# Optimization experiments

Hardware: AMD Instinct MI355X
Metric: run time of the kernel (lower is better)

The kernel has to match this reference:

```python
import jax, jax.numpy as jnp
import numpy as np

B, K, D = 4096, 16, 256
NUM_CODES = 512
BETA = 0.25  # commitment (activation_entropy=None path)
LN_EPS = 1e-5

def setup_inputs() -> dict:
    key = jax.random.key(0)
    ks = jax.random.split(key, 6)
    hidden = jax.random.normal(ks[0], (B, K, D), dtype=jnp.float32)
    active_mask = jax.random.randint(ks[1], (B, K), 0, 2).astype(bool)
    bound = 1.0 / NUM_CODES
    codebook = jax.random.uniform(ks[2], (NUM_CODES, D), minval=-bound, maxval=bound, dtype=jnp.float32)
    lim = 1.0 / np.sqrt(D)
    W_in = jax.random.uniform(ks[3], (D, D), minval=-lim, maxval=lim, dtype=jnp.float32)
    W_out = jax.random.uniform(ks[4], (D, D), minval=-lim, maxval=lim, dtype=jnp.float32)
    ln_gamma = jnp.ones((D,), jnp.float32)
    ln_beta = jnp.zeros((D,), jnp.float32)
    return {"hidden": hidden, "active_mask": active_mask, "codebook": codebook,
            "W_in": W_in, "W_out": W_out, "ln_gamma": ln_gamma, "ln_beta": ln_beta}

def reference(hidden, active_mask, codebook, W_in, W_out, ln_gamma, ln_beta):
    sg = jax.lax.stop_gradient
    z = jnp.einsum('bkd,ed->bke', hidden, W_in)              # proj_in (no bias)
    z_flat = z.reshape(-1, D)                                 # [B*K, D]
    # ||z - c||^2 = |z|^2 - 2 z.c + |c|^2
    dist = (jnp.sum(z_flat * z_flat, -1, keepdims=True)
            - 2.0 * z_flat @ codebook.T
            + jnp.sum(codebook * codebook, -1))               # [B*K, C]
    idx = jnp.argmin(dist, axis=-1)                           # [B*K]
    z_q = codebook[idx].reshape(z.shape)                      # gather
    vq_loss = jnp.mean((sg(z_q) - z) ** 2) + BETA * jnp.mean((z_q - sg(z)) ** 2)
    z_st = z + sg(z_q - z)                                    # straight-through
    out = jnp.einsum('bkd,ed->bke', z_st, W_out)              # proj_out
    h = hidden + active_mask[..., None].astype(jnp.float32) * out
    mu = jnp.mean(h, -1, keepdims=True)
    var = jnp.mean((h - mu) ** 2, -1, keepdims=True)
    h_comm = (h - mu) * jax.lax.rsqrt(var + LN_EPS) * ln_gamma + ln_beta
    return h_comm, vq_loss
```

## Files before the change

kernel.cpp:

```cpp
#include <hip/hip_runtime.h>

#define LN_EPS 1e-5f

typedef short bf16x8 __attribute__((ext_vector_type(8)));
typedef float f32x4  __attribute__((ext_vector_type(4)));

__device__ __forceinline__ unsigned short f2bf(float f) {
  unsigned u = __float_as_uint(f);
  u += 0x7fffu + ((u >> 16) & 1u);
  return (unsigned short)(u >> 16);
}
__device__ __forceinline__ float bf2f(unsigned short s) {
  return __uint_as_float(((unsigned)s) << 16);
}
__device__ __forceinline__ int swz(int r) { return (r ^ (r >> 2)) & 3; }

__device__ __forceinline__ bf16x8 pack8(float4 a, float4 b) {
  bf16x8 v;
  v[0] = (short)f2bf(a.x); v[1] = (short)f2bf(a.y);
  v[2] = (short)f2bf(a.z); v[3] = (short)f2bf(a.w);
  v[4] = (short)f2bf(b.x); v[5] = (short)f2bf(b.y);
  v[6] = (short)f2bf(b.z); v[7] = (short)f2bf(b.w);
  return v;
}

__device__ __forceinline__ void ldst16(const unsigned short* g, unsigned short* l) {
  __builtin_amdgcn_global_load_lds(
      (const __attribute__((address_space(1))) unsigned int*)g,
      (__attribute__((address_space(3))) unsigned int*)l, 16, 0, 0);
}

__global__ __launch_bounds__(256) void prep_kernel(
    const float* __restrict__ codebook, const float* __restrict__ W_in,
    const float* __restrict__ W_out,
    float* __restrict__ loss_acc, unsigned* __restrict__ ticket,
    float* __restrict__ c2, float* __restrict__ code_out,
    unsigned short* __restrict__ BT) {
  const int b = blockIdx.x, t = threadIdx.x;
  if (b < 32) {
    if (b == 0 && t == 0) { *loss_acc = 0.f; *ticket = 0u; }
    int e = b * 8 + (t >> 5);
    int c32 = t & 31, ks = c32 >> 2, kq = c32 & 3;
    const float* src = W_in + e * 256 + c32 * 8;
    float4 x0 = *(const float4*)src, x1 = *(const float4*)(src + 4);
    *(bf16x8*)(BT + ks * 8192 + e * 32 + ((kq ^ swz(e)) * 8)) = pack8(x0, x1);
  } else if (b < 96) {
    int code = (b - 32) * 8 + (t >> 5);
    int c32 = t & 31, ks = c32 >> 2, kq = c32 & 3;
    const float* src = codebook + code * 256 + c32 * 8;
    float4 x0 = *(const float4*)src, x1 = *(const float4*)(src + 4);
    int rl = code & 255;
    int chunk = 8 + (code >> 8) * 8 + ks;
    *(bf16x8*)(BT + chunk * 8192 + rl * 32 + ((kq ^ swz(rl)) * 8)) = pack8(x0, x1);
    float s = x0.x * x0.x + x0.y * x0.y + x0.z * x0.z + x0.w * x0.w +
              x1.x * x1.x + x1.y * x1.y + x1.z * x1.z + x1.w * x1.w;
    s += __shfl_xor(s, 1);  s += __shfl_xor(s, 2);
    s += __shfl_xor(s, 4);  s += __shfl_xor(s, 8);
    s += __shfl_xor(s, 16);
    if ((t & 31) == 0) c2[code] = s;
  } else {
    __shared__ float Cs[32][260];
    __shared__ float Ws[16][260];
    int bi = b - 96, ci = bi & 15, ei = bi >> 4;
    {
      int row = t >> 4, col = (t & 15) * 16;
      const float4* s = (const float4*)(W_out + (size_t)(ei * 16 + row) * 256 + col);
      float4* d = (float4*)&Ws[row][col];
      d[0] = s[0]; d[1] = s[1]; d[2] = s[2]; d[3] = s[3];
    }
    {
      int row = t >> 3, col = (t & 7) * 32;
      const float4* s = (const float4*)(codebook + (size_t)(ci * 32 + row) * 256 + col);
      float4* d = (float4*)&Cs[row][col];
      #pragma unroll
      for (int k = 0; k < 8; k++) d[k] = s[k];
    }
    __syncthreads();
    int c = t & 31, e0 = t >> 5;
    float a0 = 0.f, a1 = 0.f;
    #pragma unroll 4
    for (int d = 0; d < 256; d += 4) {
      float4 cv = *(const float4*)&Cs[c][d];
      float4 w0 = *(const float4*)&Ws[e0][d];
      float4 w1 = *(const float4*)&Ws[e0 + 8][d];
      a0 += cv.x * w0.x + cv.y * w0.y + cv.z * w0.z + cv.w * w0.w;
      a1 += cv.x * w1.x + cv.y * w1.y + cv.z * w1.z + cv.w * w1.w;
    }
    code_out[(size_t)(ci * 32 + c) * 256 + ei * 16 + e0]     = a0;
    code_out[(size_t)(ci * 32 + c) * 256 + ei * 16 + e0 + 8] = a1;
  }
}

__global__ __launch_bounds__(256, 2) void main_kernel(
    const float* __restrict__ hidden, const int* __restrict__ mask,
    const float* __restrict__ gamma, const float* __restrict__ beta,
    const float* __restrict__ c2g, const float* __restrict__ code_out,
    const unsigned short* __restrict__ BT,
    float* __restrict__ loss_acc, unsigned* __restrict__ ticket,
    float* __restrict__ out) {

  __shared__ unsigned short HZ[64 * 264];
  __shared__ unsigned short Bbuf[2][8192];
  __shared__ float c2s[512];
  __shared__ float z2[64];
  __shared__ float sminv[256];
  __shared__ int   sminc[256];
  __shared__ int   ridx[64];

  const int t    = threadIdx.x;
  const int lane = t & 63;
  const int w    = t >> 6;
  const int l15  = lane & 15;
  const int quad = lane >> 4;
  const int row0 = blockIdx.x * 64;

  c2s[t]       = c2g[t];
  c2s[t + 256] = c2g[t + 256];

  {
    int r = t >> 2, q4 = t & 3;
    const float* src = hidden + (size_t)(row0 + r) * 256 + q4 * 64;
    unsigned short* dst = HZ + r * 264 + q4 * 64;
    #pragma unroll
    for (int j = 0; j < 8; j++) {
      float4 x0 = *(const float4*)(src + j * 8);
      float4 x1 = *(const float4*)(src + j * 8 + 4);
      *(bf16x8*)(dst + j * 8) = pack8(x0, x1);
    }
  }
  __syncthreads();

  const f32x4 zf = {0.f, 0.f, 0.f, 0.f};
  f32x4 acc[4][4];
  #pragma unroll
  for (int i = 0; i < 4; i++)
    #pragma unroll
    for (int j = 0; j < 4; j++) acc[i][j] = zf;

  float runv[16];
  int   runc[16];
  #pragma unroll
  for (int r = 0; r < 16; r++) { runv[r] = 3.4e38f; runc[r] = 0; }

  {
    const unsigned short* g = BT + w * 2048 + lane * 8;
    unsigned short* l = &Bbuf[0][w * 2048];
    #pragma unroll
    for (int q = 0; q < 4; q++) ldst16(g + q * 512, l + q * 512);
  }

  for (int chunk = 0; chunk < 24; chunk++) {
    const int cu = chunk & 1;
    if (chunk == 8) {
      __builtin_amdgcn_s_waitcnt(0x0F70);
      __syncthreads();
      #pragma unroll
      for (int i = 0; i < 4; i++)
        #pragma unroll
        for (int j = 0; j < 4; j++)
          #pragma unroll
          for (int r = 0; r < 4; r++)
            HZ[(i * 16 + quad * 4 + r) * 264 + (w * 64 + j * 16 + l15)] =
                f2bf(acc[i][j][r]);
      __syncthreads();
      {
        int zr = t >> 2, part = t & 3;
        float s = 0.f;
        const unsigned short* zp = HZ + zr * 264 + part * 64;
        #pragma unroll
        for (int c = 0; c < 64; c += 8) {
          bf16x8 v = *(const bf16x8*)(zp + c);
          #pragma unroll
          for (int e = 0; e < 8; e++) { float f = bf2f((unsigned short)v[e]); s += f * f; }
        }
        s += __shfl_xor(s, 1);
        s += __shfl_xor(s, 2);
        if (part == 0) z2[zr] = s;
      }
      #pragma unroll
      for (int i = 0; i < 4; i++)
        #pragma unroll
        for (int j = 0; j < 4; j++) acc[i][j] = zf;
    } else {
      __builtin_amdgcn_s_waitcnt(0x0F70);
    }

    if (chunk < 23) {
      const unsigned short* g = BT + (chunk + 1) * 8192 + w * 2048 + lane * 8;
      unsigned short* l = &Bbuf[cu ^ 1][w * 2048];
      #pragma unroll
      for (int q = 0; q < 4; q++) ldst16(g + q * 512, l + q * 512);
    }

    const int ks = chunk & 7;
    bf16x8 a[4];
    #pragma unroll
    for (int i = 0; i < 4; i++)
      a[i] = *(const bf16x8*)(HZ + (i * 16 + l15) * 264 + ks * 32 + quad * 8);
    #pragma unroll
    for (int j = 0; j < 4; j++) {
      int c = w * 64 + j * 16 + l15;
      bf16x8 bb = *(const bf16x8*)(&Bbuf[cu][c * 32 + ((quad ^ swz(c)) * 8)]);
      #pragma unroll
      for (int i = 0; i < 4; i++)
        acc[i][j] = __builtin_amdgcn_mfma_f32_16x16x32_bf16(a[i], bb, acc[i][j], 0, 0, 0);
    }

    if (chunk == 15 || chunk == 23) {
      int pass = (chunk - 8) >> 3;
      #pragma unroll
      for (int i = 0; i < 4; i++)
        #pragma unroll
        for (int j = 0; j < 4; j++) {
          int code = pass * 256 + w * 64 + j * 16 + l15;
          float cc = c2s[code];
          #pragma unroll
          for (int r = 0; r < 4; r++) {
            float s = cc - 2.f * acc[i][j][r];
            int ri = i * 4 + r;
            if (s < runv[ri]) { runv[ri] = s; runc[ri] = code; }
          }
        }
      if (chunk == 15) {
        #pragma unroll
        for (int i = 0; i < 4; i++)
          #pragma unroll
          for (int j = 0; j < 4; j++) acc[i][j] = zf;
      }
    }
  }

  #pragma unroll
  for (int ri = 0; ri < 16; ri++) {
    float v = runv[ri]; int c = runc[ri];
    #pragma unroll
    for (int m = 1; m < 16; m <<= 1) {
      float ov = __shfl_xor(v, m);
      int   oc = __shfl_xor(c, m);
      if (ov < v || (ov == v && oc < c)) { v = ov; c = oc; }
    }
    if (l15 == 0) {
      int i = ri >> 2, r = ri & 3;
      int row = i * 16 + quad * 4 + r;
      sminv[w * 64 + row] = v;
      sminc[w * 64 + row] = c;
    }
  }
  __syncthreads();

  if (t < 64) {
    int row = t;
    float bv = sminv[row]; int bc = sminc[row];
    #pragma unroll
    for (int ww = 1; ww < 4; ww++) {
      float v = sminv[ww * 64 + row]; int c = sminc[ww * 64 + row];
      if (v < bv || (v == bv && c < bc)) { bv = v; bc = c; }
    }
    ridx[row] = bc;
    float dist = z2[row] + bv;
    #pragma unroll
    for (int m = 1; m < 64; m <<= 1) dist += __shfl_xor(dist, m);
    if (t == 0) {
      atomicAdd(loss_acc, dist);
      __threadfence();
      unsigned done = atomicAdd(ticket, 1u);
      if (done == gridDim.x - 1) {
        float total = atomicAdd(loss_acc, 0.f);
        out[16777216] = 1.25f * total * (1.f / 16777216.f);
      }
    }
  }
  __syncthreads();

  {
    float4 g4 = *(const float4*)(gamma + lane * 4);
    float4 b4 = *(const float4*)(beta + lane * 4);
    for (int rr = 0; rr < 16; rr++) {
      int row = w * 16 + rr;
      int gr  = row0 + row;
      float4 h = *(const float4*)(hidden + (size_t)gr * 256 + lane * 4);
      int code = ridx[row];
      float4 o = *(const float4*)(code_out + (size_t)code * 256 + lane * 4);
      float mf = mask[gr] ? 1.f : 0.f;
      h.x += mf * o.x; h.y += mf * o.y; h.z += mf * o.z; h.w += mf * o.w;
      float s  = h.x + h.y + h.z + h.w;
      float sq = h.x * h.x + h.y * h.y + h.z * h.z + h.w * h.w;
      #pragma unroll
      for (int m = 1; m < 64; m <<= 1) { s += __shfl_xor(s, m); sq += __shfl_xor(sq, m); }
      float mean = s * (1.f / 256.f);
      float var  = sq * (1.f / 256.f) - mean * mean;
      float rstd = rsqrtf(var + LN_EPS);
      float4 res;
      res.x = (h.x - mean) * rstd * g4.x + b4.x;
      res.y = (h.y - mean) * rstd * g4.y + b4.y;
      res.z = (h.z - mean) * rstd * g4.z + b4.z;
      res.w = (h.w - mean) * rstd * g4.w + b4.w;
      *(float4*)(out + (size_t)gr * 256 + lane * 4) = res;
    }
  }
}

extern "C" void kernel_launch(void* const* d_in, const int* in_sizes, int n_in,
                              void* d_out, int out_size, void* d_ws, size_t ws_size,
                              hipStream_t stream) {
  (void)in_sizes; (void)n_in; (void)out_size; (void)ws_size;
  const float* hidden   = (const float*)d_in[0];
  const int*   mask     = (const int*)d_in[1];
  const float* codebook = (const float*)d_in[2];
  const float* W_in     = (const float*)d_in[3];
  const float* W_out    = (const float*)d_in[4];
  const float* gamma    = (const float*)d_in[5];
  const float* beta     = (const float*)d_in[6];
  float* out = (float*)d_out;

  float* wsf      = (float*)d_ws;
  float* loss_acc = wsf;
  unsigned* ticket = (unsigned*)(wsf + 1);
  float* c2       = wsf + 64;
  float* code_out = wsf + 64 + 512;
  unsigned short* BT = (unsigned short*)(wsf + 64 + 512 + 512 * 256);

  prep_kernel<<<352, 256, 0, stream>>>(codebook, W_in, W_out, loss_acc, ticket,
                                       c2, code_out, BT);
  main_kernel<<<1024, 256, 0, stream>>>(hidden, mask, gamma, beta, c2, code_out,
                                        BT, loss_acc, ticket, out);
}
```

Measured before the change: 209.5 us.

## Load B fragments directly from global, pack argmin keys, raise occupancy

Removes the LDS double-buffered B staging (global_load_lds) and instead lays out BT so each lane reads its MFMA B fragment directly from global/L2 memory. This frees LDS and lets launch bounds request three blocks per SIMD. The argmin is also changed to a packed sortable-uint key, with the code index in the low 9 bits, reduced with plain min. Codebook norms now live in registers, and the hidden tile load is coalesced. The packed key truncates the distance mantissa, which can change tie-breaking and the loss slightly, and direct global B loads lose the explicit prefetch overlap.

```diff
diff --git a/kernel.cpp b/kernel.cpp
--- a/kernel.cpp
+++ b/kernel.cpp
@@ -13,7 +13,6 @@
 __device__ __forceinline__ float bf2f(unsigned short s) {
   return __uint_as_float(((unsigned)s) << 16);
 }
-__device__ __forceinline__ int swz(int r) { return (r ^ (r >> 2)) & 3; }
 
 __device__ __forceinline__ bf16x8 pack8(float4 a, float4 b) {
   bf16x8 v;
@@ -22,12 +21,6 @@
   v[4] = (short)f2bf(b.x); v[5] = (short)f2bf(b.y);
   v[6] = (short)f2bf(b.z); v[7] = (short)f2bf(b.w);
   return v;
-}
-
-__device__ __forceinline__ void ldst16(const unsigned short* g, unsigned short* l) {
-  __builtin_amdgcn_global_load_lds(
-      (const __attribute__((address_space(1))) unsigned int*)g,
-      (__attribute__((address_space(3))) unsigned int*)l, 16, 0, 0);
 }
 
 __global__ __launch_bounds__(256) void prep_kernel(
@@ -43,15 +36,17 @@
     int c32 = t & 31, ks = c32 >> 2, kq = c32 & 3;
     const float* src = W_in + e * 256 + c32 * 8;
     float4 x0 = *(const float4*)src, x1 = *(const float4*)(src + 4);
-    *(bf16x8*)(BT + ks * 8192 + e * 32 + ((kq ^ swz(e)) * 8)) = pack8(x0, x1);
+    *(bf16x8*)(BT + ks * 8192 + (e >> 6) * 2048 + ((e >> 4) & 3) * 512 +
+               kq * 128 + (e & 15) * 8) = pack8(x0, x1);
   } else if (b < 96) {
     int code = (b - 32) * 8 + (t >> 5);
     int c32 = t & 31, ks = c32 >> 2, kq = c32 & 3;
     const float* src = codebook + code * 256 + c32 * 8;
     float4 x0 = *(const float4*)src, x1 = *(const float4*)(src + 4);
-    int rl = code & 255;
+    int cl = code & 255;
     int chunk = 8 + (code >> 8) * 8 + ks;
-    *(bf16x8*)(BT + chunk * 8192 + rl * 32 + ((kq ^ swz(rl)) * 8)) = pack8(x0, x1);
+    *(bf16x8*)(BT + chunk * 8192 + (cl >> 6) * 2048 + ((cl >> 4) & 3) * 512 +
+               kq * 128 + (cl & 15) * 8) = pack8(x0, x1);
     float s = x0.x * x0.x + x0.y * x0.y + x0.z * x0.z + x0.w * x0.w +
               x1.x * x1.x + x1.y * x1.y + x1.z * x1.z + x1.w * x1.w;
     s += __shfl_xor(s, 1);  s += __shfl_xor(s, 2);
@@ -91,7 +86,7 @@
   }
 }
 
-__global__ __launch_bounds__(256, 2) void main_kernel(
+__global__ __launch_bounds__(256, 3) void main_kernel(
     const float* __restrict__ hidden, const int* __restrict__ mask,
     const float* __restrict__ gamma, const float* __restrict__ beta,
     const float* __restrict__ c2g, const float* __restrict__ code_out,
@@ -100,12 +95,9 @@
     float* __restrict__ out) {
 
   __shared__ unsigned short HZ[64 * 264];
-  __shared__ unsigned short Bbuf[2][8192];
-  __shared__ float c2s[512];
-  __shared__ float z2[64];
-  __shared__ float sminv[256];
-  __shared__ int   sminc[256];
-  __shared__ int   ridx[64];
+  __shared__ float    z2[64];
+  __shared__ unsigned sminp[256];
+  __shared__ int      ridx[64];
 
   const int t    = threadIdx.x;
   const int lane = t & 63;
@@ -114,18 +106,21 @@
   const int quad = lane >> 4;
   const int row0 = blockIdx.x * 64;
 
-  c2s[t]       = c2g[t];
-  c2s[t + 256] = c2g[t + 256];
+  float ccp[2][4];
+  #pragma unroll
+  for (int p = 0; p < 2; p++)
+    #pragma unroll
+    for (int j = 0; j < 4; j++)
+      ccp[p][j] = c2g[p * 256 + w * 64 + j * 16 + l15];
 
   {
-    int r = t >> 2, q4 = t & 3;
-    const float* src = hidden + (size_t)(row0 + r) * 256 + q4 * 64;
-    unsigned short* dst = HZ + r * 264 + q4 * 64;
-    #pragma unroll
-    for (int j = 0; j < 8; j++) {
-      float4 x0 = *(const float4*)(src + j * 8);
-      float4 x1 = *(const float4*)(src + j * 8 + 4);
-      *(bf16x8*)(dst + j * 8) = pack8(x0, x1);
+    #pragma unroll
+    for (int i = 0; i < 8; i++) {
+      int flat = (t * 8) + i * 2048;
+      int r = flat >> 8, c = flat & 255;
+      const float* src = hidden + (size_t)row0 * 256 + flat;
+      float4 x0 = *(const float4*)src, x1 = *(const float4*)(src + 4);
+      *(bf16x8*)(HZ + r * 264 + c) = pack8(x0, x1);
     }
   }
   __syncthreads();
@@ -137,127 +132,124 @@
     #pragma unroll
     for (int j = 0; j < 4; j++) acc[i][j] = zf;
 
-  float runv[16];
-  int   runc[16];
-  #pragma unroll
-  for (int r = 0; r < 16; r++) { runv[r] = 3.4e38f; runc[r] = 0; }
-
-  {
-    const unsigned short* g = BT + w * 2048 + lane * 8;
-    unsigned short* l = &Bbuf[0][w * 2048];
-    #pragma unroll
-    for (int q = 0; q < 4; q++) ldst16(g + q * 512, l + q * 512);
-  }
-
-  for (int chunk = 0; chunk < 24; chunk++) {
-    const int cu = chunk & 1;
-    if (chunk == 8) {
-      __builtin_amdgcn_s_waitcnt(0x0F70);
-      __syncthreads();
-      #pragma unroll
-      for (int i = 0; i < 4; i++)
-        #pragma unroll
-        for (int j = 0; j < 4; j++)
-          #pragma unroll
-          for (int r = 0; r < 4; r++)
-            HZ[(i * 16 + quad * 4 + r) * 264 + (w * 64 + j * 16 + l15)] =
-                f2bf(acc[i][j][r]);
-      __syncthreads();
-      {
-        int zr = t >> 2, part = t & 3;
-        float s = 0.f;
-        const unsigned short* zp = HZ + zr * 264 + part * 64;
-        #pragma unroll
-        for (int c = 0; c < 64; c += 8) {
-          bf16x8 v = *(const bf16x8*)(zp + c);
-          #pragma unroll
-          for (int e = 0; e < 8; e++) { float f = bf2f((unsigned short)v[e]); s += f * f; }
-        }
-        s += __shfl_xor(s, 1);
-        s += __shfl_xor(s, 2);
-        if (part == 0) z2[zr] = s;
-      }
-      #pragma unroll
-      for (int i = 0; i < 4; i++)
-        #pragma unroll
-        for (int j = 0; j < 4; j++) acc[i][j] = zf;
-    } else {
-      __builtin_amdgcn_s_waitcnt(0x0F70);
-    }
-
-    if (chunk < 23) {
-      const unsigned short* g = BT + (chunk + 1) * 8192 + w * 2048 + lane * 8;
-      unsigned short* l = &Bbuf[cu ^ 1][w * 2048];
-      #pragma unroll
-      for (int q = 0; q < 4; q++) ldst16(g + q * 512, l + q * 512);
-    }
-
-    const int ks = chunk & 7;
+  const unsigned short* BTw = BT + w * 2048 + lane * 8;
+  #pragma unroll 2
+  for (int ks = 0; ks < 8; ks++) {
+    const unsigned short* bp = BTw + ks * 8192;
+    bf16x8 b0 = *(const bf16x8*)(bp);
+    bf16x8 b1 = *(const bf16x8*)(bp + 512);
+    bf16x8 b2 = *(const bf16x8*)(bp + 1024);
+    bf16x8 b3 = *(const bf16x8*)(bp + 1536);
     bf16x8 a[4];
     #pragma unroll
     for (int i = 0; i < 4; i++)
       a[i] = *(const bf16x8*)(HZ + (i * 16 + l15) * 264 + ks * 32 + quad * 8);
     #pragma unroll
-    for (int j = 0; j < 4; j++) {
-      int c = w * 64 + j * 16 + l15;
-      bf16x8 bb = *(const bf16x8*)(&Bbuf[cu][c * 32 + ((quad ^ swz(c)) * 8)]);
+    for (int i = 0; i < 4; i++) {
+      acc[i][0] = __builtin_amdgcn_mfma_f32_16x16x32_bf16(a[i], b0, acc[i][0], 0, 0, 0);
+      acc[i][1] = __builtin_amdgcn_mfma_f32_16x16x32_bf16(a[i], b1, acc[i][1], 0, 0, 0);
+      acc[i][2] = __builtin_amdgcn_mfma_f32_16x16x32_bf16(a[i], b2, acc[i][2], 0, 0, 0);
+      acc[i][3] = __builtin_amdgcn_mfma_f32_16x16x32_bf16(a[i], b3, acc[i][3], 0, 0, 0);
+    }
+  }
+
+  __syncthreads();
+  #pragma unroll
+  for (int i = 0; i < 4; i++)
+    #pragma unroll
+    for (int j = 0; j < 4; j++)
+      #pragma unroll
+      for (int r = 0; r < 4; r++)
+        HZ[(i * 16 + quad * 4 + r) * 264 + (w * 64 + j * 16 + l15)] =
+            f2bf(acc[i][j][r]);
+  __syncthreads();
+
+  {
+    int zr = t >> 2, part = t & 3;
+    float s = 0.f;
+    const unsigned short* zp = HZ + zr * 264 + part * 64;
+    #pragma unroll
+    for (int c = 0; c < 64; c += 8) {
+      bf16x8 v = *(const bf16x8*)(zp + c);
+      #pragma unroll
+      for (int e = 0; e < 8; e++) { float f = bf2f((unsigned short)v[e]); s += f * f; }
+    }
+    s += __shfl_xor(s, 1);
+    s += __shfl_xor(s, 2);
+    if (part == 0) z2[zr] = s;
+  }
+
+  unsigned runp[16];
+  #pragma unroll
+  for (int r = 0; r < 16; r++) runp[r] = 0xFFFFFFFFu;
+
+  for (int pass = 0; pass < 2; pass++) {
+    #pragma unroll
+    for (int i = 0; i < 4; i++)
+      #pragma unroll
+      for (int j = 0; j < 4; j++) acc[i][j] = zf;
+
+    #pragma unroll 2
+    for (int ks = 0; ks < 8; ks++) {
+      const unsigned short* bp = BTw + (8 + pass * 8 + ks) * 8192;
+      bf16x8 b0 = *(const bf16x8*)(bp);
+      bf16x8 b1 = *(const bf16x8*)(bp + 512);
+      bf16x8 b2 = *(const bf16x8*)(bp + 1024);
+      bf16x8 b3 = *(const bf16x8*)(bp + 1536);
+      bf16x8 a[4];
       #pragma unroll
       for (int i = 0; i < 4; i++)
-        acc[i][j] = __builtin_amdgcn_mfma_f32_16x16x32_bf16(a[i], bb, acc[i][j], 0, 0, 0);
-    }
-
-    if (chunk == 15 || chunk == 23) {
-      int pass = (chunk - 8) >> 3;
-      #pragma unroll
-      for (int i = 0; i < 4; i++)
+        a[i] = *(const bf16x8*)(HZ + (i * 16 + l15) * 264 + ks * 32 + quad * 8);
+      #pragma unroll
+      for (int i = 0; i < 4; i++) {
+        acc[i][0] = __builtin_amdgcn_mfma_f32_16x16x32_bf16(a[i], b0, acc[i][0], 0, 0, 0);
+        acc[i][1] = __builtin_amdgcn_mfma_f32_16x16x32_bf16(a[i], b1, acc[i][1], 0, 0, 0);
+        acc[i][2] = __builtin_amdgcn_mfma_f32_16x16x32_bf16(a[i], b2, acc[i][2], 0, 0, 0);
+        acc[i][3] = __builtin_amdgcn_mfma_f32_16x16x32_bf16(a[i], b3, acc[i][3], 0, 0, 0);
+      }
+    }
+    #pragma unroll
+    for (int i = 0; i < 4; i++)
+      #pragma unroll
+      for (int j = 0; j < 4; j++) {
+        int code = pass * 256 + w * 64 + j * 16 + l15;
+        float cc = ccp[pass][j];
         #pragma unroll
-        for (int j = 0; j < 4; j++) {
-          int code = pass * 256 + w * 64 + j * 16 + l15;
-          float cc = c2s[code];
-          #pragma unroll
-          for (int r = 0; r < 4; r++) {
-            float s = cc - 2.f * acc[i][j][r];
-            int ri = i * 4 + r;
-            if (s < runv[ri]) { runv[ri] = s; runc[ri] = code; }
-          }
+        for (int r = 0; r < 4; r++) {
+          float m = cc - 2.f * acc[i][j][r];
+          unsigned bits = __float_as_uint(m);
+          unsigned u = bits ^ (0x80000000u | (unsigned)((int)bits >> 31));
+          unsigned p = (u & 0xFFFFFE00u) | (unsigned)code;
+          int ri = i * 4 + r;
+          runp[ri] = min(runp[ri], p);
         }
-      if (chunk == 15) {
-        #pragma unroll
-        for (int i = 0; i < 4; i++)
-          #pragma unroll
-          for (int j = 0; j < 4; j++) acc[i][j] = zf;
       }
-    }
   }
 
   #pragma unroll
   for (int ri = 0; ri < 16; ri++) {
-    float v = runv[ri]; int c = runc[ri];
-    #pragma unroll
-    for (int m = 1; m < 16; m <<= 1) {
-      float ov = __shfl_xor(v, m);
-      int   oc = __shfl_xor(c, m);
-      if (ov < v || (ov == v && oc < c)) { v = ov; c = oc; }
-    }
+    unsigned v = runp[ri];
+    v = min(v, (unsigned)__shfl_xor((int)v, 1));
+    v = min(v, (unsigned)__shfl_xor((int)v, 2));
+    v = min(v, (unsigned)__shfl_xor((int)v, 4));
+    v = min(v, (unsigned)__shfl_xor((int)v, 8));
     if (l15 == 0) {
       int i = ri >> 2, r = ri & 3;
-      int row = i * 16 + quad * 4 + r;
-      sminv[w * 64 + row] = v;
-      sminc[w * 64 + row] = c;
+      sminp[w * 64 + (i * 16 + quad * 4 + r)] = v;
     }
   }
   __syncthreads();
 
   if (t < 64) {
     int row = t;
-    float bv = sminv[row]; int bc = sminc[row];
-    #pragma unroll
-    for (int ww = 1; ww < 4; ww++) {
-      float v = sminv[ww * 64 + row]; int c = sminc[ww * 64 + row];
-      if (v < bv || (v == bv && c < bc)) { bv = v; bc = c; }
-    }
-    ridx[row] = bc;
-    float dist = z2[row] + bv;
+    unsigned bv = sminp[row];
+    bv = min(bv, sminp[64 + row]);
+    bv = min(bv, sminp[128 + row]);
+    bv = min(bv, sminp[192 + row]);
+    ridx[row] = (int)(bv & 511u);
+    unsigned u = bv & 0xFFFFFE00u;
+    unsigned bits = (u & 0x80000000u) ? (u ^ 0x80000000u) : ~u;
+    float dist = z2[row] + __uint_as_float(bits);
     #pragma unroll
     for (int m = 1; m < 64; m <<= 1) dist += __shfl_xor(dist, m);
     if (t == 0) {
```

Result: faster. 196.5 us (-6.2%).
